# Optimization experiments

Measured on AMD Instinct MI355X. Metric: run time of the kernel, lower is better.

The kernel has to match this reference:

```python
import jax, jax.numpy as jnp
import numpy as np

TEMPERATURE = 0.05
BETA = 1.0
LAMBDA_THRESHOLD = 0.7


def setup_inputs() -> dict:
    key = jax.random.key(0)
    k1, k2 = jax.random.split(key)
    B, D = 8192, 256
    features = jax.random.normal(k1, (B, D), dtype=jnp.float32)
    labels = jax.random.randint(k2, (B,), 0, 100, dtype=jnp.int64)
    return {"features": features, "labels": labels}


def reference(features, labels):
    B = features.shape[0]
    eps = 1e-12
    # L2 normalize rows
    f = features / jnp.maximum(jnp.linalg.norm(features, axis=1, keepdims=True), eps)
    sim = jnp.matmul(f, f.T) / TEMPERATURE                      # [B, B]
    sim_max = jnp.max(sim, axis=1, keepdims=True)               # [B, 1]
    sim_stable = sim - sim_max

    same = (labels[:, None] == labels[None, :])
    eye = jnp.eye(B, dtype=bool)
    pos_mask = same & ~eye                                       # [B, B] bool

    # Denominator: logsumexp over all non-self entries per row
    exp_sim = jnp.exp(sim_stable) * (~eye)
    log_denom = jnp.log(jnp.sum(exp_sim, axis=1, keepdims=True) + eps) + sim_max  # [B,1]

    # SCL term: mean over positive pairs of (log_denom[i] - sim[i,j])
    pos_f = pos_mask.astype(sim.dtype)
    n_pos = jnp.sum(pos_f)
    scl_sum = jnp.sum(pos_f * (log_denom - sim))
    scl_loss = jnp.where(n_pos > 0, scl_sum / jnp.maximum(n_pos, 1.0), 0.0)

    # Relaxation term: per row, logsumexp over high-sim positive logits + baseline
    high = (sim * TEMPERATURE > LAMBDA_THRESHOLD) & pos_mask     # [B, B] bool
    neg_inf = jnp.asarray(-jnp.inf, sim.dtype)
    masked_logits = jnp.where(high, sim_stable, neg_inf)          # [B, B]
    baseline = (1.0 / TEMPERATURE) - sim_max                      # [B, 1]
    all_logits = jnp.concatenate([masked_logits, baseline], axis=1)  # [B, B+1]
    row_lse = jax.nn.logsumexp(all_logits, axis=1)                # [B]
    row_has = jnp.any(high, axis=1)
    n_high = jnp.sum(high.astype(sim.dtype))
    relax_sum = jnp.sum(jnp.where(row_has, row_lse, 0.0))
    relaxation_loss = jnp.where(n_high > 0, relax_sum / jnp.maximum(n_high, 1.0), 0.0)

    total = scl_loss + BETA * relaxation_loss
    return jnp.clip(total, 0.0, 10.0)
```

## Files before the change

kernel.cpp:

```cpp
#include <hip/hip_runtime.h>
#include <hip/hip_bf16.h>
#include <math.h>

#define B_N 8192
#define D_K 256
#define TILE 128
#define NT 512
#define NBLK 64
#define NPAIR 2080
#define NCLS 100
#define KEXP 28.8539008177792681f

typedef __attribute__((ext_vector_type(8))) short short8;
typedef __attribute__((ext_vector_type(4))) float f32x4;

__device__ __forceinline__ unsigned short f2bf(float x) {
    unsigned int u = __float_as_uint(x);
    unsigned int r = (u + 0x7FFFu + ((u >> 16) & 1u)) >> 16;
    return (unsigned short)r;
}

__device__ __forceinline__ void gload_lds16(const short* g, short* l) {
    __builtin_amdgcn_global_load_lds(
        (const __attribute__((address_space(1))) void*)g,
        (__attribute__((address_space(3))) void*)l, 16, 0, 0);
}

__device__ __forceinline__ float row_sum16(float v) {
    v += __int_as_float(__builtin_amdgcn_update_dpp(0, __float_as_int(v), 0xB1, 0xF, 0xF, true));
    v += __int_as_float(__builtin_amdgcn_update_dpp(0, __float_as_int(v), 0x4E, 0xF, 0xF, true));
    v += __int_as_float(__builtin_amdgcn_update_dpp(0, __float_as_int(v), 0x141, 0xF, 0xF, true));
    v += __int_as_float(__builtin_amdgcn_update_dpp(0, __float_as_int(v), 0x140, 0xF, 0xF, true));
    return v;
}

__global__ void prep_kernel(const float* __restrict__ feat, unsigned short* __restrict__ fnorm,
                            const int* __restrict__ labels, int* __restrict__ cnt,
                            float* __restrict__ gscal, double* __restrict__ accum,
                            unsigned int* __restrict__ done) {
    if (blockIdx.x == 0) {
        __shared__ int h[NCLS];
        int t = threadIdx.x;
        if (t < NCLS) h[t] = 0;
        if (t == 0) {
            gscal[0] = 0.f; gscal[1] = 0.f;
            accum[0] = 0.0; accum[1] = 0.0; accum[2] = 0.0;
            *done = 0u;
        }
        __syncthreads();
        for (int r = t; r < B_N; r += 256) atomicAdd(&h[labels[r]], 1);
        __syncthreads();
        if (t < NCLS) cnt[t] = h[t];
    }
    int wave = threadIdx.x >> 6, lane = threadIdx.x & 63;
    int row = blockIdx.x * 4 + wave;
    float4 v = *(const float4*)(feat + (size_t)row * D_K + lane * 4);
    float ss = v.x * v.x + v.y * v.y + v.z * v.z + v.w * v.w;
    #pragma unroll
    for (int off = 1; off < 64; off <<= 1) ss += __shfl_xor(ss, off);
    float inv = 1.0f / fmaxf(sqrtf(ss), 1e-12f);
    ushort4 o;
    o.x = f2bf(v.x * inv); o.y = f2bf(v.y * inv);
    o.z = f2bf(v.z * inv); o.w = f2bf(v.w * inv);
    *(ushort4*)(fnorm + (size_t)row * D_K + lane * 4) = o;
}

__global__ __launch_bounds__(NT, 4) void main_kernel(
        const unsigned short* __restrict__ fnorm, const int* __restrict__ labels,
        float2* __restrict__ G, float* __restrict__ gscal) {
    int bid = blockIdx.x;
    int b = (int)((sqrtf(8.0f * bid + 1.0f) - 1.0f) * 0.5f);
    while ((b + 1) * (b + 2) / 2 <= bid) ++b;
    while (b * (b + 1) / 2 > bid) --b;
    int a = bid - b * (b + 1) / 2;
    const int row0 = a * TILE, col0 = b * TILE;
    const bool diag = (a == b);

    __shared__ short As[2][TILE * 64];
    __shared__ short Bs[2][TILE * 64];
    __shared__ int Ls[2 * TILE];
    __shared__ int ghs[8];
    __shared__ float gps[8];

    const int tid = threadIdx.x;
    const int lane = tid & 63, wave = tid >> 6;
    const int wm = wave >> 2, wn = wave & 3;
    const int l15 = lane & 15, lhi = lane >> 4;
    const short* fn = (const short*)fnorm;

    const int id0 = tid, id1 = tid + NT;
    const int r0s = id0 >> 3, c0s = (id0 & 7) ^ (r0s & 7), u0 = (id0 & ~63) * 8;
    const int r1s = id1 >> 3, c1s = (id1 & 7) ^ (r1s & 7), u1 = (id1 & ~63) * 8;

    if (tid < 128) Ls[tid] = labels[row0 + tid];
    else if (tid < 256) Ls[tid] = labels[col0 + tid - 128];
    if (lane == 0) ghs[wave] = 0;

    {
        gload_lds16(fn + (size_t)(row0 + r0s) * D_K + c0s * 8, &As[0][u0]);
        gload_lds16(fn + (size_t)(row0 + r1s) * D_K + c1s * 8, &As[0][u1]);
        if (!diag) {
            gload_lds16(fn + (size_t)(col0 + r0s) * D_K + c0s * 8, &Bs[0][u0]);
            gload_lds16(fn + (size_t)(col0 + r1s) * D_K + c1s * 8, &Bs[0][u1]);
        }
    }

    f32x4 acc[4][2];
    #pragma unroll
    for (int i = 0; i < 4; i++)
        #pragma unroll
        for (int j = 0; j < 2; j++) acc[i][j] = {0.f, 0.f, 0.f, 0.f};

    #pragma unroll
    for (int kc = 0; kc < 4; ++kc) {
        const int cur = kc & 1;
        __syncthreads();
        if (kc < 3) {
            const int nxt = cur ^ 1, ko = (kc + 1) * 64;
            gload_lds16(fn + (size_t)(row0 + r0s) * D_K + ko + c0s * 8, &As[nxt][u0]);
            gload_lds16(fn + (size_t)(row0 + r1s) * D_K + ko + c1s * 8, &As[nxt][u1]);
            if (!diag) {
                gload_lds16(fn + (size_t)(col0 + r0s) * D_K + ko + c0s * 8, &Bs[nxt][u0]);
                gload_lds16(fn + (size_t)(col0 + r1s) * D_K + ko + c1s * 8, &Bs[nxt][u1]);
            }
        }
        const short* Asrc = As[cur];
        const short* Bsrc = diag ? As[cur] : Bs[cur];
        #pragma unroll
        for (int ks = 0; ks < 2; ++ks) {
            short8 af[4], bfr[2];
            #pragma unroll
            for (int mi = 0; mi < 4; mi++) {
                int row = wm * 64 + mi * 16 + l15;
                int ch = (ks * 4 + lhi) ^ (l15 & 7);
                af[mi] = *(const short8*)&Asrc[row * 64 + ch * 8];
            }
            #pragma unroll
            for (int ni = 0; ni < 2; ni++) {
                int row = wn * 32 + ni * 16 + l15;
                int ch = (ks * 4 + lhi) ^ (l15 & 7);
                bfr[ni] = *(const short8*)&Bsrc[row * 64 + ch * 8];
            }
            #pragma unroll
            for (int mi = 0; mi < 4; mi++)
                #pragma unroll
                for (int ni = 0; ni < 2; ni++)
                    acc[mi][ni] = __builtin_amdgcn_mfma_f32_16x16x32_bf16(af[mi], bfr[ni], acc[mi][ni], 0, 0, 0);
        }
    }
    __syncthreads();

    float2* Rbuf = (float2*)As[0];
    float2* Cbuf = (float2*)Bs[0];

    int lc[2], colg[2];
    #pragma unroll
    for (int ni = 0; ni < 2; ni++) {
        int c = wn * 32 + ni * 16 + l15;
        lc[ni] = Ls[128 + c];
        colg[ni] = col0 + c;
    }

    float cD[2] = {0.f, 0.f};
    float gp = 0.f;
    unsigned int hmask = 0;

    #pragma unroll
    for (int mi = 0; mi < 4; mi++) {
        #pragma unroll
        for (int reg = 0; reg < 4; reg++) {
            int rloc = wm * 64 + mi * 16 + lhi * 4 + reg;
            int rowg = row0 + rloc;
            int lr = Ls[rloc];
            float d = 0.f;
            #pragma unroll
            for (int ni = 0; ni < 2; ni++) {
                float dot = acc[mi][ni][reg];
                float e = __builtin_exp2f((dot - 1.0f) * KEXP);
                bool ns = (rowg != colg[ni]);
                float ev = ns ? e : 0.f;
                d += ev; cD[ni] += ev;
                bool ps = ns && (lr == lc[ni]);
                gp += ps ? dot : 0.f;
                bool hi = ps && (dot > 0.7f);
                hmask |= hi ? (1u << ((mi * 4 + reg) * 2 + ni)) : 0u;
            }
            d = row_sum16(d);
            if (l15 == 0) Rbuf[wn * 128 + rloc] = {d, 0.f};
        }
    }

    if (!diag) {
        #pragma unroll
        for (int ni = 0; ni < 2; ni++) {
            cD[ni] += __shfl_xor(cD[ni], 16);
            cD[ni] += __shfl_xor(cD[ni], 32);
        }
        if (lhi == 0) {
            #pragma unroll
            for (int ni = 0; ni < 2; ni++)
                Cbuf[wm * 128 + wn * 32 + ni * 16 + l15] = {cD[ni], 0.f};
        }
    }

    gp = row_sum16(gp);
    gp += __shfl_xor(gp, 16);
    gp += __shfl_xor(gp, 32);
    if (lane == 0) gps[wave] = gp;

    if (__any(hmask != 0)) {
        float cR[2] = {0.f, 0.f};
        #pragma unroll
        for (int mi = 0; mi < 4; mi++) {
            #pragma unroll
            for (int reg = 0; reg < 4; reg++) {
                int rloc = wm * 64 + mi * 16 + lhi * 4 + reg;
                float rx = 0.f;
                #pragma unroll
                for (int ni = 0; ni < 2; ni++) {
                    if (hmask & (1u << ((mi * 4 + reg) * 2 + ni))) {
                        float e = __builtin_exp2f((acc[mi][ni][reg] - 1.0f) * KEXP);
                        rx += e; cR[ni] += e;
                    }
                }
                rx = row_sum16(rx);
                if (l15 == 0) Rbuf[wn * 128 + rloc].y = rx;
            }
        }
        if (!diag) {
            #pragma unroll
            for (int ni = 0; ni < 2; ni++) {
                cR[ni] += __shfl_xor(cR[ni], 16);
                cR[ni] += __shfl_xor(cR[ni], 32);
            }
            if (lhi == 0) {
                #pragma unroll
                for (int ni = 0; ni < 2; ni++)
                    Cbuf[wm * 128 + wn * 32 + ni * 16 + l15].y = cR[ni];
            }
        }
        int nhi = __popc(hmask);
        #pragma unroll
        for (int off = 1; off < 64; off <<= 1) nhi += __shfl_xor(nhi, off);
        if (lane == 0) ghs[wave] = nhi;
    }
    __syncthreads();

    if (tid < 128) {
        int r = tid;
        float2 a0 = Rbuf[r], a1 = Rbuf[128 + r], a2 = Rbuf[256 + r], a3 = Rbuf[384 + r];
        G[(size_t)b * B_N + row0 + r] = {a0.x + a1.x + a2.x + a3.x, a0.y + a1.y + a2.y + a3.y};
    } else if (tid < 256 && !diag) {
        int c = tid - 128;
        float2 a0 = Cbuf[c], a1 = Cbuf[128 + c];
        G[(size_t)a * B_N + col0 + c] = {a0.x + a1.x, a0.y + a1.y};
    }
    if (tid == 0) {
        float w = diag ? 1.0f : 2.0f;
        float gpt = gps[0] + gps[1] + gps[2] + gps[3] + gps[4] + gps[5] + gps[6] + gps[7];
        atomicAdd(&gscal[0], w * gpt);
        int tot = ghs[0] + ghs[1] + ghs[2] + ghs[3] + ghs[4] + ghs[5] + ghs[6] + ghs[7];
        if (tot > 0) atomicAdd(&gscal[1], w * (float)tot);
    }
}

__global__ void finalize_kernel(const float2* __restrict__ G, const int* __restrict__ labels,
                                const int* __restrict__ cnt, const float* __restrict__ gscal,
                                double* __restrict__ accum, unsigned int* __restrict__ done,
                                float* __restrict__ out) {
    int lane = threadIdx.x & 63, q = threadIdx.x >> 6;
    int r = blockIdx.x * 64 + lane;
    float d = 0.f, rx = 0.f;
    #pragma unroll
    for (int s = 0; s < 16; ++s) {
        float2 g = G[(size_t)(q * 16 + s) * B_N + r];
        d += g.x; rx += g.y;
    }
    __shared__ float2 sh[4][64];
    sh[q][lane] = {d, rx};
    __syncthreads();
    if (threadIdx.x < 64) {
        int rr = blockIdx.x * 64 + threadIdx.x;
        float2 t0 = sh[0][threadIdx.x], t1 = sh[1][threadIdx.x];
        float2 t2 = sh[2][threadIdx.x], t3 = sh[3][threadIdx.x];
        float dd = t0.x + t1.x + t2.x + t3.x;
        float rr2 = t0.y + t1.y + t2.y + t3.y;
        float np = (float)(cnt[labels[rr]] - 1);
        float ld = logf(dd + 1e-12f) + 20.0f;
        double s1 = (double)np * (double)ld;
        double s2 = (double)np;
        double s3 = (rr2 > 0.f) ? (double)logf(rr2 + 1.0f) : 0.0;
        #pragma unroll
        for (int off = 1; off < 64; off <<= 1) {
            s1 += __shfl_xor(s1, off);
            s2 += __shfl_xor(s2, off);
            s3 += __shfl_xor(s3, off);
        }
        if (threadIdx.x == 0) {
            atomicAdd(&accum[0], s1);
            atomicAdd(&accum[1], s2);
            atomicAdd(&accum[2], s3);
            __threadfence();
            unsigned int tk = atomicAdd(done, 1u);
            if (tk == gridDim.x - 1) {
                double a1 = atomicAdd(&accum[0], 0.0);
                double a2 = atomicAdd(&accum[1], 0.0);
                double a3 = atomicAdd(&accum[2], 0.0);
                double gp = (double)gscal[0];
                double gh = (double)gscal[1];
                double scl = (a2 > 0.0) ? (a1 - 20.0 * gp) / fmax(a2, 1.0) : 0.0;
                double rel = (gh > 0.0) ? a3 / fmax(gh, 1.0) : 0.0;
                double tot = scl + rel;
                tot = fmin(fmax(tot, 0.0), 10.0);
                out[0] = (float)tot;
            }
        }
    }
}

extern "C" void kernel_launch(void* const* d_in, const int* in_sizes, int n_in,
                              void* d_out, int out_size, void* d_ws, size_t ws_size,
                              hipStream_t stream) {
    const float* feat = (const float*)d_in[0];
    const int* labels = (const int*)d_in[1];
    float* out = (float*)d_out;
    char* ws = (char*)d_ws;

    unsigned short* fnorm = (unsigned short*)(ws);
    float2* G          = (float2*)(ws + (size_t)4 * 1024 * 1024);
    int*    cnt        = (int*)(ws + (size_t)8 * 1024 * 1024);
    float*  gscal      = (float*)(ws + (size_t)8 * 1024 * 1024 + 1024);
    double* accum      = (double*)(ws + (size_t)8 * 1024 * 1024 + 2048);
    unsigned int* done = (unsigned int*)(ws + (size_t)8 * 1024 * 1024 + 3072);

    prep_kernel<<<B_N / 4, 256, 0, stream>>>(feat, fnorm, labels, cnt, gscal, accum, done);
    main_kernel<<<NPAIR, NT, 0, stream>>>(fnorm, labels, G, gscal);
    finalize_kernel<<<B_N / 64, 256, 0, stream>>>(G, labels, cnt, gscal, accum, done, out);
    (void)in_sizes; (void)n_in; (void)out_size; (void)ws_size;
}
```

Baseline: 122.1 us.

## Fuse finalize reduction into main kernel via per-panel completion counters

Removes the separate finalize kernel launch. Each row-panel keeps an atomic counter of completed tiles, and the block that finishes a panel's last tile reduces that panel's partial sums from G and adds them to the global accumulators. A global done counter then lets the last panel reducer compute the final loss. This trades one kernel launch and its tail for atomics, thread fences and extra serial work on the last blocks of each panel.

```diff
diff --git a/kernel.cpp b/kernel.cpp
--- a/kernel.cpp
+++ b/kernel.cpp
@@ -37,15 +37,16 @@
 __global__ void prep_kernel(const float* __restrict__ feat, unsigned short* __restrict__ fnorm,
                             const int* __restrict__ labels, int* __restrict__ cnt,
                             float* __restrict__ gscal, double* __restrict__ accum,
-                            unsigned int* __restrict__ done) {
+                            unsigned int* __restrict__ gdone, int* __restrict__ pc) {
     if (blockIdx.x == 0) {
         __shared__ int h[NCLS];
         int t = threadIdx.x;
         if (t < NCLS) h[t] = 0;
+        if (t < NBLK) pc[t] = 0;
         if (t == 0) {
             gscal[0] = 0.f; gscal[1] = 0.f;
             accum[0] = 0.0; accum[1] = 0.0; accum[2] = 0.0;
-            *done = 0u;
+            *gdone = 0u;
         }
         __syncthreads();
         for (int r = t; r < B_N; r += 256) atomicAdd(&h[labels[r]], 1);
@@ -67,7 +68,10 @@
 
 __global__ __launch_bounds__(NT, 4) void main_kernel(
         const unsigned short* __restrict__ fnorm, const int* __restrict__ labels,
-        float2* __restrict__ G, float* __restrict__ gscal) {
+        float2* __restrict__ G, float* __restrict__ gscal,
+        const int* __restrict__ cnt, double* __restrict__ accum,
+        unsigned int* __restrict__ gdone, int* __restrict__ pc,
+        float* __restrict__ out) {
     int bid = blockIdx.x;
     int b = (int)((sqrtf(8.0f * bid + 1.0f) - 1.0f) * 0.5f);
     while ((b + 1) * (b + 2) / 2 <= bid) ++b;
@@ -81,6 +85,8 @@
     __shared__ int Ls[2 * TILE];
     __shared__ int ghs[8];
     __shared__ float gps[8];
+    __shared__ int doP[2];
+    __shared__ double shd[8][3];
 
     const int tid = threadIdx.x;
     const int lane = tid & 63, wave = tid >> 6;
@@ -96,13 +102,11 @@
     else if (tid < 256) Ls[tid] = labels[col0 + tid - 128];
     if (lane == 0) ghs[wave] = 0;
 
-    {
-        gload_lds16(fn + (size_t)(row0 + r0s) * D_K + c0s * 8, &As[0][u0]);
-        gload_lds16(fn + (size_t)(row0 + r1s) * D_K + c1s * 8, &As[0][u1]);
-        if (!diag) {
-            gload_lds16(fn + (size_t)(col0 + r0s) * D_K + c0s * 8, &Bs[0][u0]);
-            gload_lds16(fn + (size_t)(col0 + r1s) * D_K + c1s * 8, &Bs[0][u1]);
-        }
+    gload_lds16(fn + (size_t)(row0 + r0s) * D_K + c0s * 8, &As[0][u0]);
+    gload_lds16(fn + (size_t)(row0 + r1s) * D_K + c1s * 8, &As[0][u1]);
+    if (!diag) {
+        gload_lds16(fn + (size_t)(col0 + r0s) * D_K + c0s * 8, &Bs[0][u0]);
+        gload_lds16(fn + (size_t)(col0 + r1s) * D_K + c1s * 8, &Bs[0][u1]);
     }
 
     f32x4 acc[4][2];
@@ -262,58 +266,83 @@
         int tot = ghs[0] + ghs[1] + ghs[2] + ghs[3] + ghs[4] + ghs[5] + ghs[6] + ghs[7];
         if (tot > 0) atomicAdd(&gscal[1], w * (float)tot);
     }
-}
-
-__global__ void finalize_kernel(const float2* __restrict__ G, const int* __restrict__ labels,
-                                const int* __restrict__ cnt, const float* __restrict__ gscal,
-                                double* __restrict__ accum, unsigned int* __restrict__ done,
-                                float* __restrict__ out) {
-    int lane = threadIdx.x & 63, q = threadIdx.x >> 6;
-    int r = blockIdx.x * 64 + lane;
-    float d = 0.f, rx = 0.f;
-    #pragma unroll
-    for (int s = 0; s < 16; ++s) {
-        float2 g = G[(size_t)(q * 16 + s) * B_N + r];
-        d += g.x; rx += g.y;
-    }
-    __shared__ float2 sh[4][64];
-    sh[q][lane] = {d, rx};
+
+    __threadfence();
     __syncthreads();
-    if (threadIdx.x < 64) {
-        int rr = blockIdx.x * 64 + threadIdx.x;
-        float2 t0 = sh[0][threadIdx.x], t1 = sh[1][threadIdx.x];
-        float2 t2 = sh[2][threadIdx.x], t3 = sh[3][threadIdx.x];
-        float dd = t0.x + t1.x + t2.x + t3.x;
-        float rr2 = t0.y + t1.y + t2.y + t3.y;
-        float np = (float)(cnt[labels[rr]] - 1);
-        float ld = logf(dd + 1e-12f) + 20.0f;
-        double s1 = (double)np * (double)ld;
-        double s2 = (double)np;
-        double s3 = (rr2 > 0.f) ? (double)logf(rr2 + 1.0f) : 0.0;
+    if (tid == 0) {
+        int o0 = atomicAdd(&pc[a], 1);
+        doP[0] = (o0 == NBLK - 1) ? 1 : 0;
+        int d1 = 0;
+        if (!diag) {
+            int o1 = atomicAdd(&pc[b], 1);
+            d1 = (o1 == NBLK - 1) ? 1 : 0;
+        }
+        doP[1] = d1;
+    }
+    __syncthreads();
+
+    float2* sh2 = (float2*)As[0];
+    #pragma unroll
+    for (int pi = 0; pi < 2; ++pi) {
+        if (!doP[pi]) continue;
+        int p = (pi == 0) ? a : b;
+        {
+            int rIdx = tid & 127, q = tid >> 7;
+            int row = p * TILE + rIdx;
+            float dsum = 0.f, rxsum = 0.f;
+            #pragma unroll
+            for (int s = 0; s < 16; ++s) {
+                float2 g = G[(size_t)(q * 16 + s) * B_N + row];
+                dsum += g.x; rxsum += g.y;
+            }
+            sh2[q * 128 + rIdx] = {dsum, rxsum};
+        }
+        __syncthreads();
+        double s1 = 0.0, s2 = 0.0, s3 = 0.0;
+        if (tid < 128) {
+            float2 t0 = sh2[tid], t1 = sh2[128 + tid], t2 = sh2[256 + tid], t3 = sh2[384 + tid];
+            float dd = t0.x + t1.x + t2.x + t3.x;
+            float rr2 = t0.y + t1.y + t2.y + t3.y;
+            int rr = p * TILE + tid;
+            float np = (float)(cnt[labels[rr]] - 1);
+            float ld = logf(dd + 1e-12f) + 20.0f;
+            s1 = (double)np * (double)ld;
+            s2 = (double)np;
+            s3 = (rr2 > 0.f) ? (double)logf(rr2 + 1.0f) : 0.0;
+        }
         #pragma unroll
         for (int off = 1; off < 64; off <<= 1) {
             s1 += __shfl_xor(s1, off);
             s2 += __shfl_xor(s2, off);
             s3 += __shfl_xor(s3, off);
         }
-        if (threadIdx.x == 0) {
-            atomicAdd(&accum[0], s1);
-            atomicAdd(&accum[1], s2);
-            atomicAdd(&accum[2], s3);
-            __threadfence();
-            unsigned int tk = atomicAdd(done, 1u);
-            if (tk == gridDim.x - 1) {
-                double a1 = atomicAdd(&accum[0], 0.0);
-                double a2 = atomicAdd(&accum[1], 0.0);
-                double a3 = atomicAdd(&accum[2], 0.0);
-                double gp = (double)gscal[0];
-                double gh = (double)gscal[1];
-                double scl = (a2 > 0.0) ? (a1 - 20.0 * gp) / fmax(a2, 1.0) : 0.0;
-                double rel = (gh > 0.0) ? a3 / fmax(gh, 1.0) : 0.0;
-                double tot = scl + rel;
-                tot = fmin(fmax(tot, 0.0), 10.0);
-                out[0] = (float)tot;
-            }
+        if (lane == 0) { shd[wave][0] = s1; shd[wave][1] = s2; shd[wave][2] = s3; }
+        __syncthreads();
+        if (tid == 0) {
+            double t1 = 0, t2 = 0, t3 = 0;
+            #pragma unroll
+            for (int w2 = 0; w2 < 8; ++w2) { t1 += shd[w2][0]; t2 += shd[w2][1]; t3 += shd[w2][2]; }
+            atomicAdd(&accum[0], t1);
+            atomicAdd(&accum[1], t2);
+            atomicAdd(&accum[2], t3);
+        }
+        __syncthreads();
+    }
+
+    int npan = doP[0] + doP[1];
+    if (npan > 0 && tid == 0) {
+        __threadfence();
+        unsigned int old = atomicAdd(gdone, (unsigned int)npan);
+        if (old + (unsigned int)npan == (unsigned int)NBLK) {
+            double a1 = atomicAdd(&accum[0], 0.0);
+            double a2 = atomicAdd(&accum[1], 0.0);
+            double a3 = atomicAdd(&accum[2], 0.0);
+            double gpv = (double)atomicAdd(&gscal[0], 0.f);
+            double ghv = (double)atomicAdd(&gscal[1], 0.f);
+            double scl = (a2 > 0.0) ? (a1 - 20.0 * gpv) / fmax(a2, 1.0) : 0.0;
+            double rel = (ghv > 0.0) ? a3 / fmax(ghv, 1.0) : 0.0;
+            double tot = fmin(fmax(scl + rel, 0.0), 10.0);
+            out[0] = (float)tot;
         }
     }
 }
@@ -327,14 +356,14 @@
     char* ws = (char*)d_ws;
 
     unsigned short* fnorm = (unsigned short*)(ws);
-    float2* G          = (float2*)(ws + (size_t)4 * 1024 * 1024);
-    int*    cnt        = (int*)(ws + (size_t)8 * 1024 * 1024);
-    float*  gscal      = (float*)(ws + (size_t)8 * 1024 * 1024 + 1024);
-    double* accum      = (double*)(ws + (size_t)8 * 1024 * 1024 + 2048);
-    unsigned int* done = (unsigned int*)(ws + (size_t)8 * 1024 * 1024 + 3072);
-
-    prep_kernel<<<B_N / 4, 256, 0, stream>>>(feat, fnorm, labels, cnt, gscal, accum, done);
-    main_kernel<<<NPAIR, NT, 0, stream>>>(fnorm, labels, G, gscal);
-    finalize_kernel<<<B_N / 64, 256, 0, stream>>>(G, labels, cnt, gscal, accum, done, out);
+    float2* G           = (float2*)(ws + (size_t)4 * 1024 * 1024);
+    int*    cnt         = (int*)(ws + (size_t)8 * 1024 * 1024);
+    float*  gscal       = (float*)(ws + (size_t)8 * 1024 * 1024 + 1024);
+    double* accum       = (double*)(ws + (size_t)8 * 1024 * 1024 + 2048);
+    unsigned int* gdone = (unsigned int*)(ws + (size_t)8 * 1024 * 1024 + 3072);
+    int*    pc          = (int*)(ws + (size_t)8 * 1024 * 1024 + 3584);
+
+    prep_kernel<<<B_N / 4, 256, 0, stream>>>(feat, fnorm, labels, cnt, gscal, accum, gdone, pc);
+    main_kernel<<<NPAIR, NT, 0, stream>>>(fnorm, labels, G, gscal, cnt, accum, gdone, pc, out);
     (void)in_sizes; (void)n_in; (void)out_size; (void)ws_size;
 }
```

Result: slower. 374.0 us (+206.3%).
